# Kernel optimization log

Hardware: AMD Instinct MI355X
Metric: run time of the kernel (lower is better)

The kernel has to match this reference:

```python
import jax, jax.numpy as jnp
import numpy as np

EMBED = 768
HEADS = 12
HEAD_DIM = EMBED // HEADS
SCALE = HEAD_DIM ** -0.5


def setup_inputs() -> dict:
    key = jax.random.key(0)
    k1, k2, k3, k4, k5 = jax.random.split(key, 5)
    x = jax.random.normal(k1, (4, 2048, EMBED), dtype=jnp.float32)
    w_qkv = jax.random.normal(k2, (EMBED, 3 * EMBED), dtype=jnp.float32) * (EMBED ** -0.5)
    b_qkv = jax.random.normal(k3, (3 * EMBED,), dtype=jnp.float32) * 0.02
    w_proj = jax.random.normal(k4, (EMBED, EMBED), dtype=jnp.float32) * (EMBED ** -0.5)
    b_proj = jax.random.normal(k5, (EMBED,), dtype=jnp.float32) * 0.02
    return {"x": x, "w_qkv": w_qkv, "b_qkv": b_qkv, "w_proj": w_proj, "b_proj": b_proj}


def reference(x, w_qkv, b_qkv, w_proj, b_proj):
    B, T, D = x.shape
    qkv = x @ w_qkv + b_qkv                      # [B, T, 3D]
    qkv = qkv.reshape(B, T, 3, HEADS, HEAD_DIM)
    qkv = jnp.transpose(qkv, (2, 0, 3, 1, 4))    # [3, B, H, T, hd]
    q, k, v = qkv[0], qkv[1], qkv[2]
    scores = jnp.einsum('bhqd,bhkd->bhqk', q, k) * SCALE
    attn = jax.nn.softmax(scores, axis=-1)       # dropout p=0.0 -> identity
    out = jnp.einsum('bhqk,bhkd->bhqd', attn, v)
    out = jnp.transpose(out, (0, 2, 1, 3)).reshape(B, T, D)
    return out @ w_proj + b_proj
```

## Files before the change

kernel.cpp:

```cpp
#include <hip/hip_runtime.h>
#include <hip/hip_bf16.h>

#define EMBED 768
#define HEADS 12
#define HD 64
#define BATCH 4
#define SEQ 2048
#define M_TOK (BATCH*SEQ)
#define N_QKV (3*EMBED)
#define SL2E 0.18033688011112042f

typedef short bf8 __attribute__((ext_vector_type(8)));
typedef float f4  __attribute__((ext_vector_type(4)));
typedef unsigned short us8 __attribute__((ext_vector_type(8)));

static __device__ inline unsigned short f2bf(float f) {
    unsigned int x = __float_as_uint(f);
    unsigned int r = (x + 0x7fffu + ((x >> 16) & 1u)) >> 16;
    return (unsigned short)r;
}

__global__ void cvt_f32_bf16(const float* __restrict__ in,
                             unsigned short* __restrict__ out, int n) {
    int i = (blockIdx.x * blockDim.x + threadIdx.x) * 4;
    if (i < n) {
        float4 v = *reinterpret_cast<const float4*>(in + i);
        ushort4 o;
        o.x = f2bf(v.x); o.y = f2bf(v.y); o.z = f2bf(v.z); o.w = f2bf(v.w);
        *reinterpret_cast<ushort4*>(out + i) = o;
    }
}

__global__ void transpose_f32_bf16(const float* __restrict__ in,
                                   unsigned short* __restrict__ out, int R, int C,
                                   float scale, int nlim) {
    __shared__ float tile[32][33];
    int c0 = blockIdx.x * 32, r0 = blockIdx.y * 32;
    int tx = threadIdx.x, ty = threadIdx.y;
    for (int i = 0; i < 32; i += 8)
        tile[ty + i][tx] = in[(size_t)(r0 + ty + i) * C + c0 + tx];
    __syncthreads();
    for (int i = 0; i < 32; i += 8) {
        int orow = c0 + ty + i;
        float s = (orow < nlim) ? scale : 1.0f;
        out[(size_t)orow * R + r0 + tx] = f2bf(tile[tx][ty + i] * s);
    }
}

__global__ void scale_bias(const float* __restrict__ in, float* __restrict__ out) {
    int i = blockIdx.x * 256 + threadIdx.x;
    if (i < N_QKV) out[i] = in[i] * (i < 768 ? SL2E : 1.0f);
}

template<int OUT_MODE>
__global__ __launch_bounds__(256) void gemm_bf16(
    const unsigned short* __restrict__ A,
    const unsigned short* __restrict__ BT,
    const float* __restrict__ bias,
    void* __restrict__ Cout, int M, int N, int K)
{
    const int LDA = 40;
    __shared__ unsigned short a_lds[128 * 40];
    __shared__ unsigned short b_lds[128 * 40];
    int tid  = threadIdx.x;
    int lane = tid & 63, w = tid >> 6;
    int quad = lane >> 4, cc = lane & 15;
    int m0 = blockIdx.x * 128, n0 = blockIdx.y * 128;
    int wr = w >> 1, wc = w & 1;
    int mb = wr * 64, nb = wc * 64;
    f4 acc[4][4] = {};
    for (int k0 = 0; k0 < K; k0 += 32) {
        __syncthreads();
        for (int p = 0; p < 2; ++p) {
            int li  = p * 256 + tid;
            int row = li >> 2, ch = li & 3;
            *reinterpret_cast<uint4*>(&a_lds[row * LDA + ch * 8]) =
                *reinterpret_cast<const uint4*>(A + (size_t)(m0 + row) * K + k0 + ch * 8);
            *reinterpret_cast<uint4*>(&b_lds[row * LDA + ch * 8]) =
                *reinterpret_cast<const uint4*>(BT + (size_t)(n0 + row) * K + k0 + ch * 8);
        }
        __syncthreads();
        bf8 af[4], bfv[4];
        for (int mi = 0; mi < 4; ++mi)
            af[mi] = *reinterpret_cast<const bf8*>(&a_lds[(mb + mi * 16 + cc) * LDA + quad * 8]);
        for (int ni = 0; ni < 4; ++ni)
            bfv[ni] = *reinterpret_cast<const bf8*>(&b_lds[(nb + ni * 16 + cc) * LDA + quad * 8]);
        for (int mi = 0; mi < 4; ++mi)
            for (int ni = 0; ni < 4; ++ni)
                acc[mi][ni] = __builtin_amdgcn_mfma_f32_16x16x32_bf16(af[mi], bfv[ni], acc[mi][ni], 0, 0, 0);
    }
    for (int mi = 0; mi < 4; ++mi)
        for (int ni = 0; ni < 4; ++ni) {
            int gn = n0 + nb + ni * 16 + cc;
            float bv = bias[gn];
            for (int r = 0; r < 4; ++r) {
                int gm = m0 + mb + mi * 16 + quad * 4 + r;
                float v = acc[mi][ni][r] + bv;
                if (OUT_MODE == 0)
                    ((unsigned short*)Cout)[(size_t)gm * N + gn] = f2bf(v);
                else
                    ((float*)Cout)[(size_t)gm * N + gn] = v;
            }
        }
}

__global__ __launch_bounds__(256) void vtrans(
    const unsigned short* __restrict__ qkv, unsigned short* __restrict__ vt)
{
    __shared__ unsigned short lds[64 * 72];
    int tid = threadIdx.x;
    int t0 = blockIdx.x * 64, h = blockIdx.y, b = blockIdx.z;
    for (int p = 0; p < 2; ++p) {
        int li = p * 256 + tid, row = li >> 3, col = li & 7;
        *reinterpret_cast<uint4*>(&lds[row * 72 + col * 8]) =
            *reinterpret_cast<const uint4*>(
                qkv + (size_t)(b * SEQ + t0 + row) * 2304 + 1536 + h * 64 + col * 8);
    }
    __syncthreads();
    for (int p = 0; p < 2; ++p) {
        int li = p * 256 + tid, d = li >> 3, tc = li & 7;
        us8 v;
        for (int j = 0; j < 8; ++j) v[j] = lds[(tc * 8 + j) * 72 + d];
        *reinterpret_cast<us8*>(
            vt + ((size_t)(b * HEADS + h) * 64 + d) * SEQ + t0 + tc * 8) = v;
    }
}

__global__ __launch_bounds__(256, 4) void attn_kernel(
    const unsigned short* __restrict__ qkv,
    const unsigned short* __restrict__ vt,
    unsigned short* __restrict__ out)
{
    const int LDK = 72;
    __shared__ unsigned short k_lds[64 * 72];
    __shared__ unsigned short v_lds[64 * 72];
    __shared__ unsigned short p_lds[128 * 72];
    int tid  = threadIdx.x;
    int lane = tid & 63, w = tid >> 6;
    int quad = lane >> 4, cc = lane & 15;
    int qt = blockIdx.x, h = blockIdx.y, b = blockIdx.z;
    int q0 = qt * 128;

    bf8 qf[2][2];
    for (int nf = 0; nf < 2; ++nf) {
        const unsigned short* qp =
            qkv + (size_t)(b * SEQ + q0 + w * 32 + nf * 16 + cc) * 2304 + h * 64;
        qf[nf][0] = *reinterpret_cast<const bf8*>(qp + quad * 8);
        qf[nf][1] = *reinterpret_cast<const bf8*>(qp + 32 + quad * 8);
    }
    f4 acc[2][4] = {};
    float lsum[2] = {0.f, 0.f};
    const unsigned short* kbase = qkv + (size_t)b * SEQ * 2304 + 768 + h * 64;
    const unsigned short* vbase = vt + (size_t)(b * HEADS + h) * 64 * SEQ;

    for (int kt = 0; kt < SEQ; kt += 64) {
        __syncthreads();
        for (int p = 0; p < 2; ++p) {
            int c   = p * 256 + tid;
            int row = c >> 3, col = c & 7;
            *reinterpret_cast<uint4*>(&k_lds[row * LDK + col * 8]) =
                *reinterpret_cast<const uint4*>(kbase + (size_t)(kt + row) * 2304 + col * 8);
            *reinterpret_cast<uint4*>(&v_lds[row * LDK + col * 8]) =
                *reinterpret_cast<const uint4*>(vbase + (size_t)row * SEQ + kt + col * 8);
        }
        __syncthreads();
        for (int mt = 0; mt < 4; ++mt) {
            bf8 a0 = *reinterpret_cast<const bf8*>(&k_lds[(mt * 16 + cc) * LDK + quad * 8]);
            bf8 a1 = *reinterpret_cast<const bf8*>(&k_lds[(mt * 16 + cc) * LDK + 32 + quad * 8]);
            for (int nf = 0; nf < 2; ++nf) {
                f4 z = {};
                z = __builtin_amdgcn_mfma_f32_16x16x32_bf16(a0, qf[nf][0], z, 0, 0, 0);
                z = __builtin_amdgcn_mfma_f32_16x16x32_bf16(a1, qf[nf][1], z, 0, 0, 0);
                float p0 = exp2f(z[0]), p1 = exp2f(z[1]), p2 = exp2f(z[2]), p3 = exp2f(z[3]);
                lsum[nf] += (p0 + p1) + (p2 + p3);
                ushort4 pk; pk.x = f2bf(p0); pk.y = f2bf(p1); pk.z = f2bf(p2); pk.w = f2bf(p3);
                int ql = w * 32 + nf * 16 + cc;
                *reinterpret_cast<ushort4*>(&p_lds[ql * LDK + mt * 16 + quad * 4]) = pk;
            }
        }
        __syncthreads();
        bf8 vb0[4], vb1[4];
        for (int nt = 0; nt < 4; ++nt) {
            vb0[nt] = *reinterpret_cast<const bf8*>(&v_lds[(nt * 16 + cc) * LDK + quad * 8]);
            vb1[nt] = *reinterpret_cast<const bf8*>(&v_lds[(nt * 16 + cc) * LDK + 32 + quad * 8]);
        }
        for (int mf = 0; mf < 2; ++mf) {
            int ql = w * 32 + mf * 16 + cc;
            bf8 a0 = *reinterpret_cast<const bf8*>(&p_lds[ql * LDK + quad * 8]);
            bf8 a1 = *reinterpret_cast<const bf8*>(&p_lds[ql * LDK + 32 + quad * 8]);
            for (int nt = 0; nt < 4; ++nt) {
                acc[mf][nt] = __builtin_amdgcn_mfma_f32_16x16x32_bf16(a0, vb0[nt], acc[mf][nt], 0, 0, 0);
                acc[mf][nt] = __builtin_amdgcn_mfma_f32_16x16x32_bf16(a1, vb1[nt], acc[mf][nt], 0, 0, 0);
            }
        }
    }
    for (int nf = 0; nf < 2; ++nf) {
        lsum[nf] += __shfl_xor(lsum[nf], 16);
        lsum[nf] += __shfl_xor(lsum[nf], 32);
    }
    for (int mf = 0; mf < 2; ++mf)
        for (int r = 0; r < 4; ++r) {
            float L = __shfl(lsum[mf], quad * 4 + r);
            float inv = 1.0f / L;
            int q = q0 + w * 32 + mf * 16 + quad * 4 + r;
            size_t ob = (size_t)(b * SEQ + q) * 768 + h * 64;
            for (int nt = 0; nt < 4; ++nt)
                out[ob + nt * 16 + cc] = f2bf(acc[mf][nt][r] * inv);
        }
}

extern "C" void kernel_launch(void* const* d_in, const int* in_sizes, int n_in,
                              void* d_out, int out_size, void* d_ws, size_t ws_size,
                              hipStream_t stream) {
    const float* x      = (const float*)d_in[0];
    const float* w_qkv  = (const float*)d_in[1];
    const float* b_qkv  = (const float*)d_in[2];
    const float* w_proj = (const float*)d_in[3];
    const float* b_proj = (const float*)d_in[4];
    float* out = (float*)d_out;
    char* ws = (char*)d_ws;
    unsigned short* qkv    = (unsigned short*)(ws);
    unsigned short* vt_buf = (unsigned short*)(ws + 37748736);
    unsigned short* aout   = (unsigned short*)(ws + 50331648);
    unsigned short* xbf    = aout;
    unsigned short* wqkvT  = (unsigned short*)(ws + 62914560);
    unsigned short* wprojT = (unsigned short*)(ws + 66453504);
    float*          bqkv_s = (float*)(ws + 67633152);

    cvt_f32_bf16<<<(M_TOK * EMBED) / 1024, 256, 0, stream>>>(x, xbf, M_TOK * EMBED);
    transpose_f32_bf16<<<dim3(N_QKV / 32, EMBED / 32), dim3(32, 8), 0, stream>>>(
        w_qkv, wqkvT, EMBED, N_QKV, SL2E, 768);
    transpose_f32_bf16<<<dim3(EMBED / 32, EMBED / 32), dim3(32, 8), 0, stream>>>(
        w_proj, wprojT, EMBED, EMBED, 1.0f, 0);
    scale_bias<<<9, 256, 0, stream>>>(b_qkv, bqkv_s);
    gemm_bf16<0><<<dim3(M_TOK / 128, N_QKV / 128), 256, 0, stream>>>(
        xbf, wqkvT, bqkv_s, qkv, M_TOK, N_QKV, EMBED);
    vtrans<<<dim3(SEQ / 64, HEADS, BATCH), 256, 0, stream>>>(qkv, vt_buf);
    attn_kernel<<<dim3(SEQ / 128, HEADS, BATCH), 256, 0, stream>>>(qkv, vt_buf, aout);
    gemm_bf16<1><<<dim3(M_TOK / 128, EMBED / 128), 256, 0, stream>>>(
        aout, wprojT, b_proj, out, M_TOK, EMBED, EMBED);
}
```

Before: 265.2 us.

## Use direct global-to-LDS loads in GEMM, swizzle attention grid, drop barrier

The GEMM tile loads now use global_load_lds to copy straight into LDS, removing the padded layout so rows are contiguous. The attention launch becomes a 1D grid with a swizzled mapping that groups blocks sharing the same batch/head for better K/V cache reuse. P packing uses a hardware bf16 pack convert, and the barrier between writing and reading P is removed since each wave reads only its own rows. Removing LDS padding risks bank conflicts on fragment reads.

```diff
diff --git a/kernel.cpp b/kernel.cpp
--- a/kernel.cpp
+++ b/kernel.cpp
@@ -19,6 +19,27 @@
     unsigned int r = (x + 0x7fffu + ((x >> 16) & 1u)) >> 16;
     return (unsigned short)r;
 }
+
+static __device__ inline unsigned int pack2bf(float a, float b) {
+#if defined(__has_builtin)
+#if __has_builtin(__builtin_amdgcn_cvt_pk_bf16_f32)
+    auto r = __builtin_amdgcn_cvt_pk_bf16_f32(a, b);
+    return __builtin_bit_cast(unsigned int, r);
+#else
+    unsigned int ua = (__float_as_uint(a) + 0x8000u) >> 16;
+    unsigned int ub = (__float_as_uint(b) + 0x8000u) & 0xffff0000u;
+    return ua | ub;
+#endif
+#else
+    unsigned int ua = (__float_as_uint(a) + 0x8000u) >> 16;
+    unsigned int ub = (__float_as_uint(b) + 0x8000u) & 0xffff0000u;
+    return ua | ub;
+#endif
+}
+
+#define GLD_LDS(gp, lp) __builtin_amdgcn_global_load_lds( \
+    (const __attribute__((address_space(1))) void*)(gp),  \
+    (__attribute__((address_space(3))) void*)(lp), 16, 0, 0)
 
 __global__ void cvt_f32_bf16(const float* __restrict__ in,
                              unsigned short* __restrict__ out, int n) {
@@ -59,25 +80,25 @@
     const float* __restrict__ bias,
     void* __restrict__ Cout, int M, int N, int K)
 {
-    const int LDA = 40;
-    __shared__ unsigned short a_lds[128 * 40];
-    __shared__ unsigned short b_lds[128 * 40];
+    const int LDA = 32;
+    __shared__ unsigned short a_lds[128 * 32];
+    __shared__ unsigned short b_lds[128 * 32];
     int tid  = threadIdx.x;
     int lane = tid & 63, w = tid >> 6;
     int quad = lane >> 4, cc = lane & 15;
     int m0 = blockIdx.x * 128, n0 = blockIdx.y * 128;
     int wr = w >> 1, wc = w & 1;
     int mb = wr * 64, nb = wc * 64;
+    const unsigned short* Ab = A + (size_t)m0 * K;
+    const unsigned short* Bb = BT + (size_t)n0 * K;
     f4 acc[4][4] = {};
     for (int k0 = 0; k0 < K; k0 += 32) {
         __syncthreads();
         for (int p = 0; p < 2; ++p) {
             int li  = p * 256 + tid;
             int row = li >> 2, ch = li & 3;
-            *reinterpret_cast<uint4*>(&a_lds[row * LDA + ch * 8]) =
-                *reinterpret_cast<const uint4*>(A + (size_t)(m0 + row) * K + k0 + ch * 8);
-            *reinterpret_cast<uint4*>(&b_lds[row * LDA + ch * 8]) =
-                *reinterpret_cast<const uint4*>(BT + (size_t)(n0 + row) * K + k0 + ch * 8);
+            GLD_LDS(Ab + (size_t)row * K + k0 + ch * 8, &a_lds[li * 8]);
+            GLD_LDS(Bb + (size_t)row * K + k0 + ch * 8, &b_lds[li * 8]);
         }
         __syncthreads();
         bf8 af[4], bfv[4];
@@ -138,8 +159,12 @@
     int tid  = threadIdx.x;
     int lane = tid & 63, w = tid >> 6;
     int quad = lane >> 4, cc = lane & 15;
-    int qt = blockIdx.x, h = blockIdx.y, b = blockIdx.z;
-    int q0 = qt * 128;
+    int id  = blockIdx.x;
+    int sub = id >> 3, rem = id & 7;
+    int g   = (sub >> 4) * 8 + rem;
+    int qt  = sub & 15;
+    int b   = g / HEADS, h = g % HEADS;
+    int q0  = qt * 128;
 
     bf8 qf[2][2];
     for (int nf = 0; nf < 2; ++nf) {
@@ -173,12 +198,13 @@
                 z = __builtin_amdgcn_mfma_f32_16x16x32_bf16(a1, qf[nf][1], z, 0, 0, 0);
                 float p0 = exp2f(z[0]), p1 = exp2f(z[1]), p2 = exp2f(z[2]), p3 = exp2f(z[3]);
                 lsum[nf] += (p0 + p1) + (p2 + p3);
-                ushort4 pk; pk.x = f2bf(p0); pk.y = f2bf(p1); pk.z = f2bf(p2); pk.w = f2bf(p3);
+                uint2 pk;
+                pk.x = pack2bf(p0, p1);
+                pk.y = pack2bf(p2, p3);
                 int ql = w * 32 + nf * 16 + cc;
-                *reinterpret_cast<ushort4*>(&p_lds[ql * LDK + mt * 16 + quad * 4]) = pk;
+                *reinterpret_cast<uint2*>(&p_lds[ql * LDK + mt * 16 + quad * 4]) = pk;
             }
         }
-        __syncthreads();
         bf8 vb0[4], vb1[4];
         for (int nt = 0; nt < 4; ++nt) {
             vb0[nt] = *reinterpret_cast<const bf8*>(&v_lds[(nt * 16 + cc) * LDK + quad * 8]);
@@ -236,7 +262,7 @@
     gemm_bf16<0><<<dim3(M_TOK / 128, N_QKV / 128), 256, 0, stream>>>(
         xbf, wqkvT, bqkv_s, qkv, M_TOK, N_QKV, EMBED);
     vtrans<<<dim3(SEQ / 64, HEADS, BATCH), 256, 0, stream>>>(qkv, vt_buf);
-    attn_kernel<<<dim3(SEQ / 128, HEADS, BATCH), 256, 0, stream>>>(qkv, vt_buf, aout);
+    attn_kernel<<<768, 256, 0, stream>>>(qkv, vt_buf, aout);
     gemm_bf16<1><<<dim3(M_TOK / 128, EMBED / 128), 256, 0, stream>>>(
         aout, wprojT, b_proj, out, M_TOK, EMBED, EMBED);
 }
```

New measurement: 273.5 us. 3.1% more time.
